# Kernel optimization log

Measured on AMD Instinct MI355X. Metric: run time of the kernel, lower is better.

## Reference

```python
import jax, jax.numpy as jnp
import numpy as np

B = 16384
D_SUP, D_ANOM, D_IND = 1024, 128, 2048
D_IN = D_SUP + D_ANOM + D_IND  # 3200
H1, FEAT = 256, 128
DEPTH = 12            # hologram_depth
N_COND = 14           # num_conditions
CAP = 256             # hologram_capacity
INTERFERENCE_STRENGTH = 0.42
NUM_SPECTRA = 8
SPECTRAL_BOOST = 1.0 + 0.1 * NUM_SPECTRA  # 1.8


def setup_inputs() -> dict:
    key = jax.random.key(0)
    ks = jax.random.split(key, 16)
    s = lambda k, shape, scale=1.0: jax.random.normal(k, shape, dtype=jnp.float32) * scale
    inp = {
        "superposition": s(ks[0], (B, D_SUP)),
        "anomaly": s(ks[1], (B, D_ANOM)),
        "individual": s(ks[2], (B, D_IND)),
        # interference_processor: Linear(3200,256) -> ReLU -> Linear(256,128) -> ReLU
        "ip_W1": s(ks[3], (D_IN, H1), 1.0 / np.sqrt(D_IN)),
        "ip_b1": jnp.zeros((H1,), jnp.float32),
        "ip_W2": s(ks[4], (H1, FEAT), 1.0 / np.sqrt(H1)),
        "ip_b2": jnp.zeros((FEAT,), jnp.float32),
        "cons_W": s(ks[5], (DEPTH, FEAT, FEAT), 1.0 / np.sqrt(FEAT)),
        "cons_b": jnp.zeros((DEPTH, FEAT), jnp.float32),
        # 14 memory banks
        "ref_patterns": s(ks[6], (N_COND, CAP, FEAT)),
        "obj_patterns": s(ks[7], (N_COND, CAP, FEAT)),
        "ret_W": s(ks[8], (N_COND, FEAT, FEAT), 1.0 / np.sqrt(FEAT)),
        "ret_b": jnp.zeros((N_COND, FEAT), jnp.float32),
    }
    return inp


def reference(superposition, anomaly, individual, ip_W1, ip_b1, ip_W2, ip_b2,
              cons_W, cons_b, ref_patterns, obj_patterns, ret_W, ret_b):
    # combined input [B, 3200]
    x = jnp.concatenate([superposition, anomaly, individual], axis=1)
    # interference processor (dropout is identity in eval)
    h = jax.nn.relu(x @ ip_W1 + ip_b1)
    h = jax.nn.relu(h @ ip_W2 + ip_b2)  # [B, 128]

    # 12-layer memory consolidator via scan
    def step(state, wb):
        w, b = wb
        return jax.nn.relu(state @ w + b), None
    memory_state, _ = jax.lax.scan(step, h, (cons_W, cons_b))  # [B, 128]

    # All 14 banks batched: similarities [B, K, C]
    ref_sim = jnp.einsum('bd,kcd->bkc', memory_state, ref_patterns)
    obj_sim = jnp.einsum('bd,kcd->bkc', memory_state, obj_patterns)
    interference = ref_sim * obj_sim * (INTERFERENCE_STRENGTH * SPECTRAL_BOOST)

    # retrieval networks: [B, K, 128]
    retrieved = jnp.einsum('bd,kde->bke', memory_state, ret_W) + ret_b[None, :, :]

    anomaly_weight = jnp.mean(jnp.abs(anomaly), axis=1, keepdims=True)  # [B, 1]
    interference_weight = jnp.mean(interference, axis=2)                # [B, K]
    combined_weight = interference_weight + 0.3 * anomaly_weight        # [B, K]

    return retrieved * combined_weight[:, :, None]  # [B, 14, 128]
```

## Files before the change

kernel.cpp:

```cpp
#include <hip/hip_runtime.h>
#include <stdint.h>


typedef __attribute__((ext_vector_type(4))) float f32x4;
typedef __attribute__((ext_vector_type(8))) short s16x8;

#define SCALE_IW 0.002953125f

__device__ __forceinline__ ushort f2bf(float f) {
  uint32_t u = __builtin_bit_cast(uint32_t, f);
  u += 0x7fffu + ((u >> 16) & 1u);
  return (ushort)(u >> 16);
}
__device__ __forceinline__ float bf2f(ushort u) {
  return __builtin_bit_cast(float, ((uint32_t)u) << 16);
}
__device__ __forceinline__ uint pack2(float a, float b) {
  return (uint)f2bf(a) | ((uint)f2bf(b) << 16);
}
__device__ __forceinline__ void gl_lds16(const ushort* g, ushort* l) {
  __builtin_amdgcn_global_load_lds(
      (const __attribute__((address_space(1))) uint32_t*)g,
      (__attribute__((address_space(3))) uint32_t*)l, 16, 0, 0);
}
__device__ __forceinline__ f32x4 mfma16(s16x8 a, s16x8 b, f32x4 c) {
  return __builtin_amdgcn_mfma_f32_16x16x32_bf16(a, b, c, 0, 0, 0);
}

#define BARRIER_LGKM()                                                      \
  do {                                                                      \
    asm volatile("s_waitcnt lgkmcnt(0)" ::: "memory");                      \
    __builtin_amdgcn_s_barrier();                                           \
    asm volatile("" ::: "memory");                                          \
  } while (0)

__global__ __launch_bounds__(256) void k_prep_w1(const float* __restrict__ w1,
                                                 ushort* __restrict__ w1s) {
  const int ks = blockIdx.x, ch = blockIdx.y, t = threadIdx.x;
  ushort* out = w1s + ((size_t)ch * 100 + ks) * 4096;
#pragma unroll
  for (int i = 0; i < 2; ++i) {
    const int p = i * 256 + t, c = p >> 7, n = p & 127;
    float v[8];
#pragma unroll
    for (int j = 0; j < 8; ++j)
      v[j] = w1[(size_t)(ks * 32 + c * 8 + j) * 256 + ch * 128 + n];
    uint4 o;
    o.x = pack2(v[0], v[1]);
    o.y = pack2(v[2], v[3]);
    o.z = pack2(v[4], v[5]);
    o.w = pack2(v[6], v[7]);
    *(uint4*)(out + (size_t)(c * 128 + n) * 8) = o;
  }
}

__global__ __launch_bounds__(256) void k_prep_nk(const float* __restrict__ in,
                                                 ushort* __restrict__ out,
                                                 int in_slice, int out_slice) {
  const int t = threadIdx.x;
  const float* src = in + (size_t)blockIdx.y * in_slice;
  ushort* dst = out + (size_t)blockIdx.y * out_slice;
  const int cg = blockIdx.x * 2 + (t >> 7), n = t & 127;
  float v[8];
#pragma unroll
  for (int j = 0; j < 8; ++j) v[j] = src[(size_t)(cg * 8 + j) * 128 + n];
  uint4 o;
  o.x = pack2(v[0], v[1]);
  o.y = pack2(v[2], v[3]);
  o.z = pack2(v[4], v[5]);
  o.w = pack2(v[6], v[7]);
  *(uint4*)(dst + (size_t)cg * 1024 + n * 8) = o;
}

__global__ __launch_bounds__(128) void k_build_mt(const float* __restrict__ ref,
                                                  const float* __restrict__ obj,
                                                  ushort* __restrict__ ms) {
  const int k = blockIdx.y, e0 = blockIdx.x * 8, d = threadIdx.x;
  const float* rp = ref + (size_t)k * 256 * 128;
  const float* op = obj + (size_t)k * 256 * 128;
  float acc[8] = {};
  for (int c = 0; c < 256; ++c) {
    const float rv = rp[c * 128 + d];
#pragma unroll
    for (int j = 0; j < 8; ++j) acc[j] += rv * op[c * 128 + e0 + j];
  }
  ushort* o = ms + (size_t)k * 16384 + (d >> 3) * 1024 + (d & 7);
#pragma unroll
  for (int j = 0; j < 8; ++j) o[(e0 + j) * 8] = f2bf(acc[j] * SCALE_IW);
}

__global__ __launch_bounds__(256, 4) void k_gemm1(
    const float* __restrict__ sup, const float* __restrict__ anom,
    const float* __restrict__ ind, const ushort* __restrict__ w1s,
    const float* __restrict__ b1, ushort* __restrict__ h1) {
  __shared__ alignas(16) ushort As[2][32 * 40];
  __shared__ alignas(16) ushort Bs[2][4096];
  const int t = threadIdx.x;
  const int w = t >> 6, l = t & 63, m = l & 15, q = l >> 4;
  const int n0 = blockIdx.x * 128;
  const int b0 = blockIdx.y * 32;
  const int ar = t >> 3, ac = t & 7;
  const ushort* wbase = w1s + (size_t)blockIdx.x * 409600;
  f32x4 acc[2][2] = {};
  float4 xr[8];

#define XLOAD(KS, SLOT)                                                   \
  {                                                                       \
    const int k0_ = (KS) * 32;                                            \
    const float* src_;                                                    \
    int rs_, ko_;                                                         \
    if (k0_ < 1024)      { src_ = sup;  rs_ = 1024; ko_ = k0_; }          \
    else if (k0_ < 1152) { src_ = anom; rs_ = 128;  ko_ = k0_ - 1024; }   \
    else                 { src_ = ind;  rs_ = 2048; ko_ = k0_ - 1152; }   \
    xr[SLOT] =                                                            \
        *(const float4*)(src_ + (size_t)(b0 + ar) * rs_ + ko_ + ac * 4);  \
  }
#define STAGE_A(BUF, SLOT)                                    \
  {                                                           \
    uint2 pk_;                                                \
    pk_.x = pack2(xr[SLOT].x, xr[SLOT].y);                    \
    pk_.y = pack2(xr[SLOT].z, xr[SLOT].w);                    \
    *(uint2*)(As[BUF] + ar * 40 + ac * 4) = pk_;              \
  }
#define STAGE_B(KS, BUF)                                       \
  {                                                            \
    _Pragma("unroll")                                          \
    for (int i_ = 0; i_ < 2; ++i_) {                           \
      const int s_ = i_ * 256 + t;                             \
      gl_lds16(wbase + (size_t)(KS) * 4096 + s_ * 8,           \
               Bs[BUF] + s_ * 8);                              \
    }                                                          \
  }
#define COMPUTE(CUR)                                                        \
  {                                                                         \
    s16x8 af_[2], bf_[2];                                                   \
    _Pragma("unroll")                                                       \
    for (int rt = 0; rt < 2; ++rt)                                          \
      af_[rt] = *(const s16x8*)(As[CUR] + (rt * 16 + m) * 40 + q * 8);      \
    _Pragma("unroll")                                                       \
    for (int ct = 0; ct < 2; ++ct)                                          \
      bf_[ct] =                                                             \
          *(const s16x8*)(Bs[CUR] + q * 1024 + (w * 32 + ct * 16 + m) * 8); \
    _Pragma("unroll")                                                       \
    for (int rt = 0; rt < 2; ++rt)                                          \
      _Pragma("unroll")                                                     \
      for (int ct = 0; ct < 2; ++ct)                                        \
        acc[rt][ct] = mfma16(af_[rt], bf_[ct], acc[rt][ct]);                \
  }

  XLOAD(0, 0);
  STAGE_A(0, 0);
  STAGE_B(0, 0);
  XLOAD(1, 1);

  for (int g = 0; g < 12; ++g) {
    const int g8 = g * 8;
#pragma unroll
    for (int u = 0; u < 8; ++u) {
      const int ks = g8 + u;
      __syncthreads();
      const int cur = u & 1, nxt = cur ^ 1;
      STAGE_A(nxt, (u + 1) & 7);
      STAGE_B(ks + 1, nxt);
      if (u == 0) {
#pragma unroll
        for (int j = 0; j < 8; ++j) XLOAD(g8 + 2 + j, (2 + j) & 7);
      }
      COMPUTE(cur);
    }
  }
  __syncthreads();
  STAGE_A(1, 1);
  STAGE_B(97, 1);
  XLOAD(98, 2);
  XLOAD(99, 3);
  COMPUTE(0);
  __syncthreads();
  STAGE_A(0, 2);
  STAGE_B(98, 0);
  COMPUTE(1);
  __syncthreads();
  STAGE_A(1, 3);
  STAGE_B(99, 1);
  COMPUTE(0);
  __syncthreads();
  COMPUTE(1);
#undef XLOAD
#undef STAGE_A
#undef STAGE_B
#undef COMPUTE
#pragma unroll
  for (int ct = 0; ct < 2; ++ct) {
    const int col = n0 + w * 32 + ct * 16 + m;
    const float bias = b1[col];
#pragma unroll
    for (int rt = 0; rt < 2; ++rt)
#pragma unroll
      for (int r = 0; r < 4; ++r) {
        const int row = b0 + rt * 16 + q * 4 + r;
        h1[(size_t)row * 256 + col] = f2bf(fmaxf(acc[rt][ct][r] + bias, 0.f));
      }
  }
}

__global__ __launch_bounds__(256, 2) void k_cons(
    const ushort* __restrict__ h1, const ushort* __restrict__ w2s,
    const ushort* __restrict__ cws, const float* __restrict__ b2,
    const float* __restrict__ cb, ushort* __restrict__ stateg) {
  __shared__ alignas(16) ushort A0[32 * 264];
  __shared__ alignas(16) ushort S0[32 * 136];
  __shared__ alignas(16) ushort S1[32 * 136];
  __shared__ alignas(16) ushort Wh[2][8192];
  const int t = threadIdx.x;
  const int w = t >> 6, l = t & 63, m = l & 15, q = l >> 4;
  const int b0 = blockIdx.x * 32;

  auto stage = [&](int p) {
    const ushort* src = (p < 4) ? w2s + (size_t)p * 8192
                                : cws + (size_t)(p - 4) * 8192;
    ushort* dst = Wh[p & 1];
#pragma unroll
    for (int i = 0; i < 4; ++i) {
      const int s = i * 256 + t;
      gl_lds16(src + s * 8, dst + s * 8);
    }
  };

  stage(0);
#pragma unroll
  for (int i = 0; i < 4; ++i) {
    const int s = i * 256 + t, r = s >> 5, c = s & 31;
    *(uint4*)(A0 + r * 264 + c * 8) =
        *(const uint4*)(h1 + (size_t)(b0 + r) * 256 + c * 8);
  }

  f32x4 acc[2][2] = {};
  for (int p = 0; p < 28; ++p) {
    __syncthreads();
    if (p < 27) stage(p + 1);
    const int layer = (p < 4) ? 0 : 1 + ((p - 4) >> 1);
    const ushort* Asrc;
    int astr, koff;
    if (p < 4) { Asrc = A0; astr = 264; koff = p * 64; }
    else {
      Asrc = (layer & 1) ? (const ushort*)S0 : (const ushort*)S1;
      astr = 136;
      koff = ((p - 4) & 1) * 64;
    }
    const ushort* Wb = Wh[p & 1];
#pragma unroll
    for (int ksl = 0; ksl < 2; ++ksl) {
      const int cl = ksl * 4 + q;
      s16x8 af[2];
#pragma unroll
      for (int rt = 0; rt < 2; ++rt)
        af[rt] = *(const s16x8*)(Asrc + (rt * 16 + m) * astr + koff + cl * 8);
#pragma unroll
      for (int ct = 0; ct < 2; ++ct) {
        const s16x8 bf =
            *(const s16x8*)(Wb + cl * 1024 + (w * 32 + ct * 16 + m) * 8);
#pragma unroll
        for (int rt = 0; rt < 2; ++rt)
          acc[rt][ct] = mfma16(af[rt], bf, acc[rt][ct]);
      }
    }
    const bool layer_end = (p == 3) || (p >= 4 && ((p - 4) & 1));
    if (layer_end) {
      const float* bias = (layer == 0) ? b2 : cb + (layer - 1) * 128;
      ushort* dst = (layer & 1) ? S1 : S0;
#pragma unroll
      for (int ct = 0; ct < 2; ++ct) {
        const int col = w * 32 + ct * 16 + m;
        const float bv = bias[col];
#pragma unroll
        for (int rt = 0; rt < 2; ++rt)
#pragma unroll
          for (int r = 0; r < 4; ++r) {
            dst[(rt * 16 + q * 4 + r) * 136 + col] =
                f2bf(fmaxf(acc[rt][ct][r] + bv, 0.f));
            acc[rt][ct][r] = 0.f;
          }
      }
    }
  }
  __syncthreads();
  const ushort* fin = S0;
#pragma unroll
  for (int i = 0; i < 2; ++i) {
    const int s = i * 256 + t, r = s >> 4, c = s & 15;
    *(uint4*)(stateg + (size_t)(b0 + r) * 128 + c * 8) =
        *(const uint4*)(fin + r * 136 + c * 8);
  }
}

__global__ __launch_bounds__(256, 2) void k_banks(
    const ushort* __restrict__ stateg, const float* __restrict__ anom,
    const ushort* __restrict__ ms, const ushort* __restrict__ rws,
    const float* __restrict__ retb, float* __restrict__ out) {
  __shared__ alignas(16) ushort S[32 * 136];
  __shared__ alignas(16) ushort Mb[16384];
  __shared__ alignas(16) ushort Rb[16384];
  __shared__ alignas(16) float iwbuf[4][32];
  __shared__ alignas(16) float wvs[32];
  __shared__ alignas(16) float aws[32];
  const int t = threadIdx.x;
  const int w = t >> 6, l = t & 63, m = l & 15, q = l >> 4;
  const int b0 = blockIdx.x * 32;

  auto stagek = [&](int kk) {
#pragma unroll
    for (int i = 0; i < 8; ++i) {
      const int s = i * 256 + t;
      gl_lds16(ms + (size_t)kk * 16384 + s * 8, Mb + s * 8);
      gl_lds16(rws + (size_t)kk * 16384 + s * 8, Rb + s * 8);
    }
  };

  stagek(0);
#pragma unroll
  for (int i = 0; i < 2; ++i) {
    const int s = i * 256 + t, r = s >> 4, c = s & 15;
    *(uint4*)(S + r * 136 + c * 8) =
        *(const uint4*)(stateg + (size_t)(b0 + r) * 128 + c * 8);
  }
  {
    const int r = t >> 3, qq = t & 7;
    float sa = 0.f;
#pragma unroll
    for (int j = 0; j < 4; ++j) {
      const float4 v =
          *(const float4*)(anom + (size_t)(b0 + r) * 128 + qq * 16 + j * 4);
      sa += fabsf(v.x) + fabsf(v.y) + fabsf(v.z) + fabsf(v.w);
    }
    sa += __shfl_xor(sa, 1, 8);
    sa += __shfl_xor(sa, 2, 8);
    sa += __shfl_xor(sa, 4, 8);
    if (qq == 0) aws[r] = sa * (0.3f / 128.f);
  }
  __syncthreads();
  s16x8 af[4][2];
#pragma unroll
  for (int ks = 0; ks < 4; ++ks)
#pragma unroll
    for (int rt = 0; rt < 2; ++rt)
      af[ks][rt] = *(const s16x8*)(S + (rt * 16 + m) * 136 + (ks * 4 + q) * 8);
  float sc[2][4][2];
#pragma unroll
  for (int rt = 0; rt < 2; ++rt)
#pragma unroll
    for (int r = 0; r < 4; ++r)
#pragma unroll
      for (int ct = 0; ct < 2; ++ct)
        sc[rt][r][ct] =
            bf2f(S[(rt * 16 + q * 4 + r) * 136 + (w * 32 + ct * 16 + m)]);

  for (int k = 0; k < 14; ++k) {
    __syncthreads();
    f32x4 P[2][2] = {}, R[2][2] = {};
#pragma unroll
    for (int ks = 0; ks < 4; ++ks)
#pragma unroll
      for (int ct = 0; ct < 2; ++ct) {
        const int boff = (ks * 4 + q) * 1024 + (w * 32 + ct * 16 + m) * 8;
        const s16x8 bm = *(const s16x8*)(Mb + boff);
        const s16x8 br = *(const s16x8*)(Rb + boff);
#pragma unroll
        for (int rt = 0; rt < 2; ++rt) {
          P[rt][ct] = mfma16(af[ks][rt], bm, P[rt][ct]);
          R[rt][ct] = mfma16(af[ks][rt], br, R[rt][ct]);
        }
      }
#pragma unroll
    for (int rt = 0; rt < 2; ++rt) {
      float pr[4];
#pragma unroll
      for (int r = 0; r < 4; ++r) {
        float v = P[rt][0][r] * sc[rt][r][0] + P[rt][1][r] * sc[rt][r][1];
        v += __shfl_xor(v, 1, 16);
        v += __shfl_xor(v, 2, 16);
        v += __shfl_xor(v, 4, 16);
        v += __shfl_xor(v, 8, 16);
        pr[r] = v;
      }
      if (m == 0)
        *(float4*)&iwbuf[w][rt * 16 + q * 4] =
            make_float4(pr[0], pr[1], pr[2], pr[3]);
    }
    BARRIER_LGKM();
    if (k < 13) stagek(k + 1);
    if (t < 32)
      wvs[t] = iwbuf[0][t] + iwbuf[1][t] + iwbuf[2][t] + iwbuf[3][t] + aws[t];
    BARRIER_LGKM();
#pragma unroll
    for (int ct = 0; ct < 2; ++ct) {
      const int col = w * 32 + ct * 16 + m;
      const float rb = retb[k * 128 + col];
#pragma unroll
      for (int rt = 0; rt < 2; ++rt) {
        const float4 wv4 = *(const float4*)&wvs[rt * 16 + q * 4];
        const float wvv[4] = {wv4.x, wv4.y, wv4.z, wv4.w};
#pragma unroll
        for (int r = 0; r < 4; ++r) {
          const int row = b0 + rt * 16 + q * 4 + r;
          out[(size_t)row * 1792 + k * 128 + col] = wvv[r] * (R[rt][ct][r] + rb);
        }
      }
    }
  }
}

extern "C" void kernel_launch(void* const* d_in, const int* in_sizes, int n_in,
                              void* d_out, int out_size, void* d_ws,
                              size_t ws_size, hipStream_t stream) {
  const float* sup   = (const float*)d_in[0];
  const float* anom  = (const float*)d_in[1];
  const float* ind   = (const float*)d_in[2];
  const float* ipW1  = (const float*)d_in[3];
  const float* ipb1  = (const float*)d_in[4];
  const float* ipW2  = (const float*)d_in[5];
  const float* ipb2  = (const float*)d_in[6];
  const float* consW = (const float*)d_in[7];
  const float* consb = (const float*)d_in[8];
  const float* refp  = (const float*)d_in[9];
  const float* objp  = (const float*)d_in[10];
  const float* retW  = (const float*)d_in[11];
  const float* retb  = (const float*)d_in[12];
  float* out = (float*)d_out;
  char* ws = (char*)d_ws;
  ushort* W1S = (ushort*)(ws);
  ushort* W2S = (ushort*)(ws + 1638400);
  ushort* CWS = (ushort*)(ws + 1703936);
  ushort* RWS = (ushort*)(ws + 2097152);
  ushort* MS  = (ushort*)(ws + 2555904);
  ushort* H1  = (ushort*)(ws + 3014656);
  ushort* ST  = (ushort*)(ws + 11403264);

  k_prep_w1<<<dim3(100, 2), 256, 0, stream>>>(ipW1, W1S);
  k_prep_nk<<<dim3(16, 1), 256, 0, stream>>>(ipW2, W2S, 0, 0);
  k_prep_nk<<<dim3(8, 12), 256, 0, stream>>>(consW, CWS, 16384, 16384);
  k_prep_nk<<<dim3(8, 14), 256, 0, stream>>>(retW, RWS, 16384, 16384);
  k_build_mt<<<dim3(16, 14), 128, 0, stream>>>(refp, objp, MS);
  k_gemm1<<<dim3(2, 512), 256, 0, stream>>>(sup, anom, ind, W1S, ipb1, H1);
  k_cons<<<512, 256, 0, stream>>>(H1, W2S, CWS, ipb2, consb, ST);
  k_banks<<<512, 256, 0, stream>>>(ST, anom, MS, RWS, retb, out);
}
```

Baseline: 434.2 us.

## Deepen gemm1 pipeline with 4-slot weight buffers and merge prep kernels

```diff
diff --git a/kernel.cpp b/kernel.cpp
--- a/kernel.cpp
+++ b/kernel.cpp
@@ -27,6 +27,13 @@
   return __builtin_amdgcn_mfma_f32_16x16x32_bf16(a, b, c, 0, 0, 0);
 }
 
+#define FENCE() asm volatile("" ::: "memory")
+#define BARRIER_VM(N)                                                       \
+  do {                                                                      \
+    asm volatile("s_waitcnt vmcnt(" #N ") lgkmcnt(0)" ::: "memory");        \
+    __builtin_amdgcn_s_barrier();                                           \
+    asm volatile("" ::: "memory");                                          \
+  } while (0)
 #define BARRIER_LGKM()                                                      \
   do {                                                                      \
     asm volatile("s_waitcnt lgkmcnt(0)" ::: "memory");                      \
@@ -34,59 +41,73 @@
     asm volatile("" ::: "memory");                                          \
   } while (0)
 
-__global__ __launch_bounds__(256) void k_prep_w1(const float* __restrict__ w1,
-                                                 ushort* __restrict__ w1s) {
-  const int ks = blockIdx.x, ch = blockIdx.y, t = threadIdx.x;
-  ushort* out = w1s + ((size_t)ch * 100 + ks) * 4096;
-#pragma unroll
-  for (int i = 0; i < 2; ++i) {
-    const int p = i * 256 + t, c = p >> 7, n = p & 127;
+__global__ __launch_bounds__(256) void k_prep(
+    const float* __restrict__ w1, const float* __restrict__ w2,
+    const float* __restrict__ cw, const float* __restrict__ rw,
+    const float* __restrict__ ref, const float* __restrict__ obj,
+    ushort* __restrict__ w1s, ushort* __restrict__ w2s,
+    ushort* __restrict__ cws, ushort* __restrict__ rws,
+    ushort* __restrict__ ms) {
+  const int b = blockIdx.x, t = threadIdx.x;
+  if (b < 200) {
+    const int ks = b % 100, ch = b / 100;
+    ushort* out = w1s + ((size_t)ch * 100 + ks) * 4096;
+#pragma unroll
+    for (int i = 0; i < 2; ++i) {
+      const int p = i * 256 + t, c = p >> 7, n = p & 127;
+      float v[8];
+#pragma unroll
+      for (int j = 0; j < 8; ++j)
+        v[j] = w1[(size_t)(ks * 32 + c * 8 + j) * 256 + ch * 128 + n];
+      uint4 o;
+      o.x = pack2(v[0], v[1]);
+      o.y = pack2(v[2], v[3]);
+      o.z = pack2(v[4], v[5]);
+      o.w = pack2(v[6], v[7]);
+      *(uint4*)(out + (size_t)(c * 128 + n) * 8) = o;
+    }
+  } else if (b < 424) {
+    const float* src;
+    ushort* dst;
+    int bx;
+    if (b < 216) {
+      src = w2; dst = w2s; bx = b - 200;
+    } else if (b < 312) {
+      const int bb = b - 216;
+      src = cw + (size_t)(bb / 8) * 16384;
+      dst = cws + (size_t)(bb / 8) * 16384;
+      bx = bb % 8;
+    } else {
+      const int bb = b - 312;
+      src = rw + (size_t)(bb / 8) * 16384;
+      dst = rws + (size_t)(bb / 8) * 16384;
+      bx = bb % 8;
+    }
+    const int cg = bx * 2 + (t >> 7), n = t & 127;
     float v[8];
 #pragma unroll
-    for (int j = 0; j < 8; ++j)
-      v[j] = w1[(size_t)(ks * 32 + c * 8 + j) * 256 + ch * 128 + n];
+    for (int j = 0; j < 8; ++j) v[j] = src[(size_t)(cg * 8 + j) * 128 + n];
     uint4 o;
     o.x = pack2(v[0], v[1]);
     o.y = pack2(v[2], v[3]);
     o.z = pack2(v[4], v[5]);
     o.w = pack2(v[6], v[7]);
-    *(uint4*)(out + (size_t)(c * 128 + n) * 8) = o;
-  }
-}
-
-__global__ __launch_bounds__(256) void k_prep_nk(const float* __restrict__ in,
-                                                 ushort* __restrict__ out,
-                                                 int in_slice, int out_slice) {
-  const int t = threadIdx.x;
-  const float* src = in + (size_t)blockIdx.y * in_slice;
-  ushort* dst = out + (size_t)blockIdx.y * out_slice;
-  const int cg = blockIdx.x * 2 + (t >> 7), n = t & 127;
-  float v[8];
-#pragma unroll
-  for (int j = 0; j < 8; ++j) v[j] = src[(size_t)(cg * 8 + j) * 128 + n];
-  uint4 o;
-  o.x = pack2(v[0], v[1]);
-  o.y = pack2(v[2], v[3]);
-  o.z = pack2(v[4], v[5]);
-  o.w = pack2(v[6], v[7]);
-  *(uint4*)(dst + (size_t)cg * 1024 + n * 8) = o;
-}
-
-__global__ __launch_bounds__(128) void k_build_mt(const float* __restrict__ ref,
-                                                  const float* __restrict__ obj,
-                                                  ushort* __restrict__ ms) {
-  const int k = blockIdx.y, e0 = blockIdx.x * 8, d = threadIdx.x;
-  const float* rp = ref + (size_t)k * 256 * 128;
-  const float* op = obj + (size_t)k * 256 * 128;
-  float acc[8] = {};
-  for (int c = 0; c < 256; ++c) {
-    const float rv = rp[c * 128 + d];
-#pragma unroll
-    for (int j = 0; j < 8; ++j) acc[j] += rv * op[c * 128 + e0 + j];
-  }
-  ushort* o = ms + (size_t)k * 16384 + (d >> 3) * 1024 + (d & 7);
-#pragma unroll
-  for (int j = 0; j < 8; ++j) o[(e0 + j) * 8] = f2bf(acc[j] * SCALE_IW);
+    *(uint4*)(dst + (size_t)cg * 1024 + n * 8) = o;
+  } else {
+    const int bb = b - 424;
+    const int k = bb / 8, e0 = (bb % 8) * 16 + (t >> 7) * 8, d = t & 127;
+    const float* rp = ref + (size_t)k * 256 * 128;
+    const float* op = obj + (size_t)k * 256 * 128;
+    float acc[8] = {};
+    for (int c = 0; c < 256; ++c) {
+      const float rv = rp[c * 128 + d];
+#pragma unroll
+      for (int j = 0; j < 8; ++j) acc[j] += rv * op[c * 128 + e0 + j];
+    }
+    ushort* o = ms + (size_t)k * 16384 + (d >> 3) * 1024 + (d & 7);
+#pragma unroll
+    for (int j = 0; j < 8; ++j) o[(e0 + j) * 8] = f2bf(acc[j] * SCALE_IW);
+  }
 }
 
 __global__ __launch_bounds__(256, 4) void k_gemm1(
@@ -94,7 +115,7 @@
     const float* __restrict__ ind, const ushort* __restrict__ w1s,
     const float* __restrict__ b1, ushort* __restrict__ h1) {
   __shared__ alignas(16) ushort As[2][32 * 40];
-  __shared__ alignas(16) ushort Bs[2][4096];
+  __shared__ alignas(16) ushort Bs[4][4096];
   const int t = threadIdx.x;
   const int w = t >> 6, l = t & 63, m = l & 15, q = l >> 4;
   const int n0 = blockIdx.x * 128;
@@ -102,11 +123,12 @@
   const int ar = t >> 3, ac = t & 7;
   const ushort* wbase = w1s + (size_t)blockIdx.x * 409600;
   f32x4 acc[2][2] = {};
-  float4 xr[8];
+  float4 xr[16];
 
 #define XLOAD(KS, SLOT)                                                   \
   {                                                                       \
-    const int k0_ = (KS) * 32;                                            \
+    const int kc_ = (KS) > 99 ? 99 : (KS);                                \
+    const int k0_ = kc_ * 32;                                             \
     const float* src_;                                                    \
     int rs_, ko_;                                                         \
     if (k0_ < 1024)      { src_ = sup;  rs_ = 1024; ko_ = k0_; }          \
@@ -122,73 +144,90 @@
     pk_.y = pack2(xr[SLOT].z, xr[SLOT].w);                    \
     *(uint2*)(As[BUF] + ar * 40 + ac * 4) = pk_;              \
   }
-#define STAGE_B(KS, BUF)                                       \
+#define STAGE_B(KS, SLOT)                                      \
   {                                                            \
     _Pragma("unroll")                                          \
     for (int i_ = 0; i_ < 2; ++i_) {                           \
       const int s_ = i_ * 256 + t;                             \
       gl_lds16(wbase + (size_t)(KS) * 4096 + s_ * 8,           \
-               Bs[BUF] + s_ * 8);                              \
+               Bs[SLOT] + s_ * 8);                             \
     }                                                          \
   }
-#define COMPUTE(CUR)                                                        \
+#define BURST(G8, BK)                                          \
+  {                                                            \
+    _Pragma("unroll")                                          \
+    for (int j_ = 0; j_ < 8; ++j_)                             \
+      XLOAD((G8) + 8 + j_, j_ + 8 * ((BK) ^ 1));               \
+  }
+#define COMPUTE(AB, BSLOT)                                                  \
   {                                                                         \
     s16x8 af_[2], bf_[2];                                                   \
     _Pragma("unroll")                                                       \
     for (int rt = 0; rt < 2; ++rt)                                          \
-      af_[rt] = *(const s16x8*)(As[CUR] + (rt * 16 + m) * 40 + q * 8);      \
+      af_[rt] = *(const s16x8*)(As[AB] + (rt * 16 + m) * 40 + q * 8);       \
     _Pragma("unroll")                                                       \
     for (int ct = 0; ct < 2; ++ct)                                          \
       bf_[ct] =                                                             \
-          *(const s16x8*)(Bs[CUR] + q * 1024 + (w * 32 + ct * 16 + m) * 8); \
+          *(const s16x8*)(Bs[BSLOT] + q * 1024 + (w * 32 + ct * 16 + m) * 8); \
     _Pragma("unroll")                                                       \
     for (int rt = 0; rt < 2; ++rt)                                          \
       _Pragma("unroll")                                                     \
       for (int ct = 0; ct < 2; ++ct)                                        \
         acc[rt][ct] = mfma16(af_[rt], bf_[ct], acc[rt][ct]);                \
   }
-
-  XLOAD(0, 0);
+#define ITER(G8, U, BK, NLIT, XSLOT)                           \
+  {                                                            \
+    BARRIER_VM(NLIT);                                          \
+    STAGE_A(((U) + 1) & 1, XSLOT);                             \
+    if ((U) == 0) { BURST(G8, BK); FENCE(); }                  \
+    STAGE_B((G8) + (U) + 3, ((U) + 3) & 3);                    \
+    FENCE();                                                   \
+    COMPUTE((U) & 1, (U) & 3);                                 \
+  }
+#define GROUP(G8, BK)                                          \
+  ITER(G8, 0, BK, 4,  (1 + 8 * (BK)))                          \
+  ITER(G8, 1, BK, 12, (2 + 8 * (BK)))                          \
+  ITER(G8, 2, BK, 12, (3 + 8 * (BK)))                          \
+  ITER(G8, 3, BK, 4,  (4 + 8 * (BK)))                          \
+  ITER(G8, 4, BK, 4,  (5 + 8 * (BK)))                          \
+  ITER(G8, 5, BK, 4,  (6 + 8 * (BK)))                          \
+  ITER(G8, 6, BK, 4,  (7 + 8 * (BK)))                          \
+  ITER(G8, 7, BK, 4,  (8 * ((BK) ^ 1)))
+
+#pragma unroll
+  for (int j = 0; j < 8; ++j) XLOAD(j, j);
+  FENCE();
+  STAGE_B(0, 0);
+  STAGE_B(1, 1);
+  STAGE_B(2, 2);
+  FENCE();
   STAGE_A(0, 0);
-  STAGE_B(0, 0);
-  XLOAD(1, 1);
-
-  for (int g = 0; g < 12; ++g) {
-    const int g8 = g * 8;
-#pragma unroll
-    for (int u = 0; u < 8; ++u) {
-      const int ks = g8 + u;
-      __syncthreads();
-      const int cur = u & 1, nxt = cur ^ 1;
-      STAGE_A(nxt, (u + 1) & 7);
-      STAGE_B(ks + 1, nxt);
-      if (u == 0) {
-#pragma unroll
-        for (int j = 0; j < 8; ++j) XLOAD(g8 + 2 + j, (2 + j) & 7);
-      }
-      COMPUTE(cur);
-    }
-  }
-  __syncthreads();
+
+  for (int gg = 0; gg < 6; ++gg) {
+    const int h = gg * 16;
+    GROUP(h, 0)
+    GROUP(h + 8, 1)
+  }
+  BARRIER_VM(4);
   STAGE_A(1, 1);
-  STAGE_B(97, 1);
-  XLOAD(98, 2);
-  XLOAD(99, 3);
-  COMPUTE(0);
-  __syncthreads();
+  STAGE_B(99, 3);
+  FENCE();
+  COMPUTE(0, 0);
+  BARRIER_VM(4);
   STAGE_A(0, 2);
-  STAGE_B(98, 0);
-  COMPUTE(1);
-  __syncthreads();
+  COMPUTE(1, 1);
+  BARRIER_VM(2);
   STAGE_A(1, 3);
-  STAGE_B(99, 1);
-  COMPUTE(0);
-  __syncthreads();
-  COMPUTE(1);
+  COMPUTE(0, 2);
+  BARRIER_VM(0);
+  COMPUTE(1, 3);
 #undef XLOAD
 #undef STAGE_A
 #undef STAGE_B
+#undef BURST
 #undef COMPUTE
+#undef ITER
+#undef GROUP
 #pragma unroll
   for (int ct = 0; ct < 2; ++ct) {
     const int col = n0 + w * 32 + ct * 16 + m;
@@ -435,11 +474,8 @@
   ushort* H1  = (ushort*)(ws + 3014656);
   ushort* ST  = (ushort*)(ws + 11403264);
 
-  k_prep_w1<<<dim3(100, 2), 256, 0, stream>>>(ipW1, W1S);
-  k_prep_nk<<<dim3(16, 1), 256, 0, stream>>>(ipW2, W2S, 0, 0);
-  k_prep_nk<<<dim3(8, 12), 256, 0, stream>>>(consW, CWS, 16384, 16384);
-  k_prep_nk<<<dim3(8, 14), 256, 0, stream>>>(retW, RWS, 16384, 16384);
-  k_build_mt<<<dim3(16, 14), 128, 0, stream>>>(refp, objp, MS);
+  k_prep<<<536, 256, 0, stream>>>(ipW1, ipW2, consW, retW, refp, objp,
+                                  W1S, W2S, CWS, RWS, MS);
   k_gemm1<<<dim3(2, 512), 256, 0, stream>>>(sup, anom, ind, W1S, ipb1, H1);
   k_cons<<<512, 256, 0, stream>>>(H1, W2S, CWS, ipb2, consb, ST);
   k_banks<<<512, 256, 0, stream>>>(ST, anom, MS, RWS, retb, out);
```

Result: faster. 421.6 us (-2.9%).
